# Optimization experiments

Measured on AMD Instinct MI355X. Metric: run time of the kernel, lower is better.

## Reference

```python
import jax, jax.numpy as jnp
import numpy as np

L, B, D, H = 4096, 4, 1024, 16
HD = D // H
SCALAR = 700.0


def setup_inputs() -> dict:
    key = jax.random.key(0)
    ks = jax.random.split(key, 9)
    bound = np.sqrt(6.0 / (D + D)).astype(np.float32)  # xavier_uniform for square weights
    def xavier(k):
        return jax.random.uniform(k, (D, D), jnp.float32, -bound, bound)
    return {
        "input_tensor": jax.random.normal(ks[0], (L, B, D), jnp.float32),
        "num_heads": H,
        "Wq": xavier(ks[1]), "bq": jnp.zeros((D,), jnp.float32),
        "Wk": xavier(ks[2]), "bk": jnp.zeros((D,), jnp.float32),
        "Wv": xavier(ks[3]), "bv": jnp.zeros((D,), jnp.float32),
        "Wo": xavier(ks[4]), "bo": jnp.zeros((D,), jnp.float32),
        "scalar": jnp.asarray(SCALAR, jnp.float32),
    }


def reference(input_tensor, num_heads, Wq, bq, Wk, bk, Wv, bv, Wo, bo, scalar):
    l, b, d = input_tensor.shape
    h = num_heads
    hd = d // h
    scaling = hd ** -0.5
    X = jnp.transpose(input_tensor, (1, 0, 2))  # (b, l, d)
    q = (X @ Wq.T + bq) * scaling
    k = X @ Wk.T + bk
    v = X @ Wv.T + bv
    # split heads: (b, l, h*hd) -> (b, h, l, hd)
    q = q.reshape(b, l, h, hd).transpose(0, 2, 1, 3)
    k = k.reshape(b, l, h, hd).transpose(0, 2, 1, 3)
    v = v.reshape(b, l, h, hd).transpose(0, 2, 1, 3)
    # linear attention: (K^T V) then Q @ (...)  -> O(l * hd^2)
    kv = jnp.einsum('bhld,bhle->bhde', k, v)        # (b, h, hd, hd)
    out = jnp.einsum('bhld,bhde->bhle', q, kv) / scalar  # (b, h, l, hd)
    # faithful to einops '(b h) l d -> b l (d h)': feature layout is (hd, h)
    out = out.transpose(0, 2, 3, 1).reshape(b, l, d)  # (b, l, hd*h)
    out = out @ Wo.T + bo
    return jnp.transpose(out, (1, 0, 2))  # (l, b, d)
```

## Files before the change

### kernel.cpp

```cpp
#include <hip/hip_runtime.h>
#include <stdint.h>
#include <stddef.h>

typedef unsigned short ushort_t;
typedef __attribute__((ext_vector_type(8))) short short8;
typedef __attribute__((ext_vector_type(4))) float f32x4;
typedef __attribute__((ext_vector_type(4))) float float4v;

#define L_DIM 4096
#define B_DIM 4
#define D_DIM 1024
#define H_DIM 16
#define HD_DIM 64
#define M_DIM (L_DIM * B_DIM)

__device__ __forceinline__ float bf2f(ushort_t u) {
    union { unsigned int i; float f; } v; v.i = ((unsigned int)u) << 16; return v.f;
}
__device__ __forceinline__ ushort_t f2bf(float f) {
    union { float f; unsigned int i; } v; v.f = f;
    unsigned int r = v.i + 0x7FFFu + ((v.i >> 16) & 1u);
    return (ushort_t)(r >> 16);
}
__device__ __forceinline__ unsigned int pk2(float a, float b) {
    return (unsigned int)f2bf(a) | ((unsigned int)f2bf(b) << 16);
}
__device__ __forceinline__ void gload16(const ushort_t* g, ushort_t* l) {
    __builtin_amdgcn_global_load_lds(
        (const __attribute__((address_space(1))) unsigned int*)g,
        (__attribute__((address_space(3))) unsigned int*)l, 16, 0, 0);
}

__global__ void detect_kernel(const ushort_t* __restrict__ scal, int* __restrict__ flag)
{
    *flag = (scal[0] == 0) ? 1 : 0;
}

__global__ void convert_b_kernel(const void* bq, const void* bk, const void* bv,
                                 const void* bo, float* __restrict__ bias_f,
                                 const int* __restrict__ flag)
{
    int fl = *flag;
    int idx = blockIdx.x * 256 + threadIdx.x;
    int j = idx >> 10, i = idx & 1023;
    const void* p = (j == 0) ? bq : (j == 1) ? bk : (j == 2) ? bv : bo;
    bias_f[idx] = fl ? ((const float*)p)[i] : bf2f(((const ushort_t*)p)[i]);
}

__global__ void convert_w_kernel(const void* Wk, const void* Wv, const void* Wo,
                                 ushort_t* __restrict__ Wkc, ushort_t* __restrict__ Wvc,
                                 ushort_t* __restrict__ Wpc,
                                 const int* __restrict__ flag)
{
    int fl = *flag;
    int z = blockIdx.z;
    int idx = blockIdx.x * 256 + threadIdx.x;
    const void* src = (z == 0) ? Wk : (z == 1) ? Wv : Wo;
    ushort_t* dst   = (z == 0) ? Wkc : (z == 1) ? Wvc : Wpc;
    size_t sidx;
    if (z < 2) sidx = (size_t)idx;
    else {
        int n = idx >> 10, f = idx & 1023;
        int hh = f >> 6, e = f & 63;
        sidx = (size_t)n * D_DIM + e * H_DIM + hh;
    }
    dst[idx] = fl ? f2bf(((const float*)src)[sidx]) : ((const ushort_t*)src)[sidx];
}

__global__ void convert_x_kernel(const void* __restrict__ X, ushort_t* __restrict__ Xb,
                                 const int* __restrict__ flag)
{
    int fl = *flag;
    size_t i8 = ((size_t)blockIdx.x * 256 + threadIdx.x) * 8;
    if (fl) {
        const float4v* p = (const float4v*)((const float*)X + i8);
        float4v f0 = p[0], f1 = p[1];
        uint4 u;
        u.x = pk2(f0.x, f0.y); u.y = pk2(f0.z, f0.w);
        u.z = pk2(f1.x, f1.y); u.w = pk2(f1.z, f1.w);
        *(uint4*)(Xb + i8) = u;
    } else {
        *(uint4*)(Xb + i8) = *(const uint4*)((const ushort_t*)X + i8);
    }
}

__global__ __launch_bounds__(256) void proj_kernel(
    const ushort_t* __restrict__ A, int a_base0, int a_zstride, int astride,
    const ushort_t* __restrict__ W0, int w_z,
    const float* __restrict__ bias0, int b_z,
    void* __restrict__ out, int o_base0, int o_zstride, int ostride,
    const int* __restrict__ flag, int o_dyn)
{
    __shared__ ushort_t lA[128 * 32];
    __shared__ ushort_t lB[128 * 32];
    const int z    = blockIdx.z;
    const int a_base = a_base0 + z * a_zstride;
    const int o_base = o_base0 + z * o_zstride;
    const ushort_t* W = W0 + (size_t)z * w_z * (D_DIM * D_DIM);
    const float* bias = bias0 + z * b_z * D_DIM;
    const int ofl  = o_dyn & *flag;
    const int t    = threadIdx.x;
    const int m0   = blockIdx.x * 128;
    const int n0   = blockIdx.y * 128;
    const int w    = t >> 6;
    const int lane = t & 63;
    const int quad = lane >> 4;
    const int l16  = lane & 15;
    const int wm   = (w >> 1) * 64;
    const int wn   = (w & 1) * 64;

    const int c0 = t, c1 = t + 256;
    const int r0 = c0 >> 2, col0 = (c0 & 3) * 8;
    const int r1 = c1 >> 2, col1 = (c1 & 3) * 8;

    f32x4 acc[4][4];
#pragma unroll
    for (int i = 0; i < 4; i++)
#pragma unroll
        for (int j = 0; j < 4; j++) acc[i][j] = f32x4{0.f, 0.f, 0.f, 0.f};

    for (int k0 = 0; k0 < D_DIM; k0 += 32) {
        __syncthreads();
        gload16(A + (size_t)(a_base + (m0 + r0) * astride) * D_DIM + k0 + col0, &lA[c0 * 8]);
        gload16(A + (size_t)(a_base + (m0 + r1) * astride) * D_DIM + k0 + col1, &lA[c1 * 8]);
        gload16(W + (size_t)(n0 + r0) * D_DIM + k0 + col0, &lB[c0 * 8]);
        gload16(W + (size_t)(n0 + r1) * D_DIM + k0 + col1, &lB[c1 * 8]);
        __syncthreads();
        short8 af[4], bfr[4];
#pragma unroll
        for (int mt = 0; mt < 4; mt++)
            af[mt] = *(const short8*)&lA[(wm + mt * 16 + l16) * 32 + quad * 8];
#pragma unroll
        for (int nt = 0; nt < 4; nt++)
            bfr[nt] = *(const short8*)&lB[(wn + nt * 16 + l16) * 32 + quad * 8];
#pragma unroll
        for (int mt = 0; mt < 4; mt++)
#pragma unroll
            for (int nt = 0; nt < 4; nt++)
                acc[mt][nt] = __builtin_amdgcn_mfma_f32_16x16x32_bf16(
                    af[mt], bfr[nt], acc[mt][nt], 0, 0, 0);
    }

#pragma unroll
    for (int mt = 0; mt < 4; mt++) {
#pragma unroll
        for (int nt = 0; nt < 4; nt++) {
            int gn = n0 + wn + nt * 16 + l16;
            float bv = bias[gn];
#pragma unroll
            for (int i = 0; i < 4; i++) {
                int gm = m0 + wm + mt * 16 + quad * 4 + i;
                size_t oidx = (size_t)(o_base + gm * ostride) * D_DIM + gn;
                float val = acc[mt][nt][i] + bv;
                if (ofl) ((float*)out)[oidx] = val;
                else     ((ushort_t*)out)[oidx] = f2bf(val);
            }
        }
    }
}

__global__ __launch_bounds__(256) void kv_chunk_kernel(
    const ushort_t* __restrict__ kc, const ushort_t* __restrict__ vc,
    float* __restrict__ part, int lps)
{
    __shared__ ushort_t lkT[64 * 32];
    __shared__ ushort_t lvT[64 * 32];
    const int t    = threadIdx.x;
    const int s    = blockIdx.x;
    const int bh   = blockIdx.y;
    const int b    = bh >> 4, h = bh & 15;
    const int w    = t >> 6;
    const int lane = t & 63, quad = lane >> 4, l16 = lane & 15;

    f32x4 acc[4];
#pragma unroll
    for (int i = 0; i < 4; i++) acc[i] = f32x4{0.f, 0.f, 0.f, 0.f};

    const int niter = lps >> 5;
    for (int kt = 0; kt < niter; kt++) {
        int lcur = s * lps + kt * 32;
        __syncthreads();
#pragma unroll
        for (int i = 0; i < 4; i++) {
            int u  = t + 256 * i;
            int l  = u >> 5;
            int dp = u & 31;
            size_t goff = ((size_t)(lcur + l) * B_DIM + b) * D_DIM + h * HD_DIM + dp * 2;
            unsigned int kw = *(const unsigned int*)(kc + goff);
            unsigned int vw = *(const unsigned int*)(vc + goff);
            lkT[(2 * dp) * 32 + l]     = (ushort_t)kw;
            lkT[(2 * dp + 1) * 32 + l] = (ushort_t)(kw >> 16);
            lvT[(2 * dp) * 32 + l]     = (ushort_t)vw;
            lvT[(2 * dp + 1) * 32 + l] = (ushort_t)(vw >> 16);
        }
        __syncthreads();
        short8 af = *(const short8*)&lvT[(w * 16 + l16) * 32 + quad * 8];
#pragma unroll
        for (int dt = 0; dt < 4; dt++) {
            short8 bfr = *(const short8*)&lkT[(dt * 16 + l16) * 32 + quad * 8];
            acc[dt] = __builtin_amdgcn_mfma_f32_16x16x32_bf16(af, bfr, acc[dt], 0, 0, 0);
        }
    }
#pragma unroll
    for (int dt = 0; dt < 4; dt++) {
#pragma unroll
        for (int i = 0; i < 4; i++) {
            int e = w * 16 + quad * 4 + i;
            int d = dt * 16 + l16;
            part[(((size_t)s * 64 + bh) * 64 + e) * 64 + d] += acc[dt][i];
        }
    }
}

__global__ void kv_reduce_kernel(const float* __restrict__ part,
                                 ushort_t* __restrict__ kvT,
                                 const void* __restrict__ scal,
                                 const int* __restrict__ flag)
{
    int fl = *flag;
    float sc = fl ? *(const float*)scal : bf2f(((const ushort_t*)scal)[0]);
    float inv = 1.0f / sc;
    int idx = blockIdx.x * 256 + threadIdx.x;
    float sum = 0.0f;
#pragma unroll
    for (int s = 0; s < 4; s++) sum += part[((size_t)s << 18) + idx];
    kvT[idx] = f2bf(sum * inv);
}

__global__ __launch_bounds__(256) void wfuse_kernel(
    const void* __restrict__ Wq, const ushort_t* __restrict__ kvT,
    ushort_t* __restrict__ Wf, const int* __restrict__ flag)
{
    __shared__ ushort_t kvL[4096];
    const int fl = *flag;
    const int kt = blockIdx.x, h = blockIdx.y, b = blockIdx.z;
    const int t  = threadIdx.x;
    for (int i = t; i < 2048; i += 256)
        ((unsigned int*)kvL)[i] =
            ((const unsigned int*)(kvT + ((size_t)(b * 16 + h) << 12)))[i];
    __syncthreads();
    const int k  = kt * 128 + (t & 127);
    const int e0 = (t >> 7) * 32;
    float acc[32];
#pragma unroll
    for (int j = 0; j < 32; j++) acc[j] = 0.f;
    for (int d = 0; d < 64; d++) {
        size_t wi = (size_t)(h * 64 + d) * D_DIM + k;
        float wv = 0.125f * (fl ? ((const float*)Wq)[wi]
                                : bf2f(((const ushort_t*)Wq)[wi]));
#pragma unroll
        for (int j = 0; j < 32; j++)
            acc[j] += bf2f(kvL[(e0 + j) * 64 + d]) * wv;
    }
#pragma unroll
    for (int j = 0; j < 32; j++)
        Wf[((size_t)b * 1024 + h * 64 + e0 + j) * D_DIM + k] = f2bf(acc[j]);
}

__global__ void bias_fuse_kernel(const float* __restrict__ bq_f,
                                 const ushort_t* __restrict__ kvT,
                                 float* __restrict__ bfused)
{
    int idx = blockIdx.x * 256 + threadIdx.x;
    int b = idx >> 10, h = (idx >> 6) & 15, e = idx & 63;
    const ushort_t* kvp = kvT + ((size_t)(b * 16 + h) << 12) + e * 64;
    float s = 0.f;
#pragma unroll
    for (int d = 0; d < 64; d++) s += bf2f(kvp[d]) * bq_f[h * 64 + d];
    bfused[idx] = 0.125f * s;
}

extern "C" void kernel_launch(void* const* d_in, const int* in_sizes, int n_in,
                              void* d_out, int out_size, void* d_ws, size_t ws_size,
                              hipStream_t stream)
{
    const void* X    = d_in[0];
    const void* Wq   = d_in[2];
    const void* bq   = d_in[3];
    const void* Wk   = d_in[4];
    const void* bk   = d_in[5];
    const void* Wv   = d_in[6];
    const void* bv   = d_in[7];
    const void* Wo   = d_in[8];
    const void* bo   = d_in[9];
    const void* scal = d_in[10];

    char* ws = (char*)d_ws;
    int*      flag   = (int*)(ws + 0);
    float*    bias_f = (float*)(ws + 1024);
    float*    bfused = (float*)(ws + 32768);
    ushort_t* Wkc    = (ushort_t*)(ws + 65536);
    ushort_t* Wvc    = (ushort_t*)(ws + 2162688);
    ushort_t* Wpc    = (ushort_t*)(ws + 4259840);
    ushort_t* Wfused = (ushort_t*)(ws + 6356992);
    ushort_t* kvT    = (ushort_t*)(ws + 14745600);
    float*    part   = (float*)(ws + 15269888);
    ushort_t* Xb     = (ushort_t*)(ws + 19464192);
    ushort_t* kvbuf  = (ushort_t*)(ws + 53018624);
    ushort_t* kc     = kvbuf;
    ushort_t* vc     = kvbuf + (size_t)8192 * D_DIM;
    ushort_t* attnb  = kvbuf;

    detect_kernel<<<1, 1, 0, stream>>>((const ushort_t*)scal, flag);
    convert_b_kernel<<<16, 256, 0, stream>>>(bq, bk, bv, bo, bias_f, flag);
    convert_w_kernel<<<dim3(4096, 1, 3), 256, 0, stream>>>(Wk, Wv, Wo, Wkc, Wvc, Wpc, flag);
    convert_x_kernel<<<8192, 256, 0, stream>>>(X, Xb, flag);
    hipMemsetAsync(part, 0, 4194304, stream);

    for (int c = 0; c < 2; c++) {
        proj_kernel<<<dim3(64, 8, 2), 256, 0, stream>>>(
            Xb, c * 8192, 0, 1,
            Wkc, 1,
            bias_f + 1024, 1,
            kvbuf, 0, 8192, 1,
            flag, 0);
        kv_chunk_kernel<<<dim3(4, 64), 256, 0, stream>>>(kc, vc, part, 512);
    }
    kv_reduce_kernel<<<1024, 256, 0, stream>>>(part, kvT, scal, flag);

    wfuse_kernel<<<dim3(8, 16, 4), 256, 0, stream>>>(Wq, kvT, Wfused, flag);
    bias_fuse_kernel<<<16, 256, 0, stream>>>(bias_f, kvT, bfused);

    proj_kernel<<<dim3(32, 8, 4), 256, 0, stream>>>(
        Xb, 0, 1, 4,
        Wfused, 1,
        bfused, 1,
        attnb, 0, 4096, 1,
        flag, 0);

    proj_kernel<<<dim3(32, 8, 4), 256, 0, stream>>>(
        attnb, 0, 4096, 1,
        Wpc, 0,
        bias_f + 3072, 0,
        d_out, 0, 1, 4,
        flag, 1);
}
```

Before: 488.0 us.

## Fold output projection into fused Q weight, eliminating one full-size GEMM

The per-batch fused query weight (Wq scaled and combined with KV) is now multiplied by Wo up front in a small 1024x1024 per-batch GEMM. A single large projection of X then produces the output directly, with a matching fused bias computed by a new bias2 kernel. This removes one 16384x1024x1024 GEMM and the intermediate attention buffer, at the cost of a small extra weight GEMM, an extra bf16 rounding step on the combined weight, and a transposed wfuse store pattern. The KV chunk split is also doubled from 4 to 8 partial sums, with a larger partial buffer and reduction.

```diff
diff --git a/kernel.cpp b/kernel.cpp
--- a/kernel.cpp
+++ b/kernel.cpp
@@ -223,13 +223,13 @@
     int idx = blockIdx.x * 256 + threadIdx.x;
     float sum = 0.0f;
 #pragma unroll
-    for (int s = 0; s < 4; s++) sum += part[((size_t)s << 18) + idx];
+    for (int s = 0; s < 8; s++) sum += part[((size_t)s << 18) + idx];
     kvT[idx] = f2bf(sum * inv);
 }
 
 __global__ __launch_bounds__(256) void wfuse_kernel(
     const void* __restrict__ Wq, const ushort_t* __restrict__ kvT,
-    ushort_t* __restrict__ Wf, const int* __restrict__ flag)
+    ushort_t* __restrict__ WfT, const int* __restrict__ flag)
 {
     __shared__ ushort_t kvL[4096];
     const int fl = *flag;
@@ -254,7 +254,7 @@
     }
 #pragma unroll
     for (int j = 0; j < 32; j++)
-        Wf[((size_t)b * 1024 + h * 64 + e0 + j) * D_DIM + k] = f2bf(acc[j]);
+        WfT[((size_t)b * 1024 + k) * D_DIM + h * 64 + e0 + j] = f2bf(acc[j]);
 }
 
 __global__ void bias_fuse_kernel(const float* __restrict__ bq_f,
@@ -268,6 +268,20 @@
 #pragma unroll
     for (int d = 0; d < 64; d++) s += bf2f(kvp[d]) * bq_f[h * 64 + d];
     bfused[idx] = 0.125f * s;
+}
+
+__global__ void bias2_kernel(const ushort_t* __restrict__ Wpc,
+                             const float* __restrict__ bfused,
+                             const float* __restrict__ bo_f,
+                             float* __restrict__ b2)
+{
+    int idx = blockIdx.x * 256 + threadIdx.x;
+    int b = idx >> 10, n = idx & 1023;
+    const ushort_t* wr = Wpc + (size_t)n * D_DIM;
+    const float* bf = bfused + b * 1024;
+    float s = 0.f;
+    for (int f = 0; f < 1024; f++) s += bf2f(wr[f]) * bf[f];
+    b2[idx] = s + bo_f[n];
 }
 
 extern "C" void kernel_launch(void* const* d_in, const int* in_sizes, int n_in,
@@ -289,23 +303,26 @@
     int*      flag   = (int*)(ws + 0);
     float*    bias_f = (float*)(ws + 1024);
     float*    bfused = (float*)(ws + 32768);
-    ushort_t* Wkc    = (ushort_t*)(ws + 65536);
-    ushort_t* Wvc    = (ushort_t*)(ws + 2162688);
-    ushort_t* Wpc    = (ushort_t*)(ws + 4259840);
-    ushort_t* Wfused = (ushort_t*)(ws + 6356992);
-    ushort_t* kvT    = (ushort_t*)(ws + 14745600);
-    float*    part   = (float*)(ws + 15269888);
-    ushort_t* Xb     = (ushort_t*)(ws + 19464192);
-    ushort_t* kvbuf  = (ushort_t*)(ws + 53018624);
+    float*    b2     = (float*)(ws + 65536);
+    float*    bias_z = (float*)(ws + 98304);
+    ushort_t* Wkc    = (ushort_t*)(ws + 131072);
+    ushort_t* Wvc    = (ushort_t*)(ws + 2228224);
+    ushort_t* Wpc    = (ushort_t*)(ws + 4325376);
+    ushort_t* kvT    = (ushort_t*)(ws + 6422528);
+    float*    part   = (float*)(ws + 6946816);
+    ushort_t* Xb     = (ushort_t*)(ws + 15335424);
+    ushort_t* kvbuf  = (ushort_t*)(ws + 48889856);
     ushort_t* kc     = kvbuf;
     ushort_t* vc     = kvbuf + (size_t)8192 * D_DIM;
-    ushort_t* attnb  = kvbuf;
+    ushort_t* WfT    = kvbuf;
+    ushort_t* W2     = kvbuf + (size_t)4194304;
 
     detect_kernel<<<1, 1, 0, stream>>>((const ushort_t*)scal, flag);
     convert_b_kernel<<<16, 256, 0, stream>>>(bq, bk, bv, bo, bias_f, flag);
     convert_w_kernel<<<dim3(4096, 1, 3), 256, 0, stream>>>(Wk, Wv, Wo, Wkc, Wvc, Wpc, flag);
     convert_x_kernel<<<8192, 256, 0, stream>>>(X, Xb, flag);
-    hipMemsetAsync(part, 0, 4194304, stream);
+    hipMemsetAsync(part, 0, 8388608, stream);
+    hipMemsetAsync(bias_z, 0, 4096, stream);
 
     for (int c = 0; c < 2; c++) {
         proj_kernel<<<dim3(64, 8, 2), 256, 0, stream>>>(
@@ -314,24 +331,25 @@
             bias_f + 1024, 1,
             kvbuf, 0, 8192, 1,
             flag, 0);
-        kv_chunk_kernel<<<dim3(4, 64), 256, 0, stream>>>(kc, vc, part, 512);
+        kv_chunk_kernel<<<dim3(8, 64), 256, 0, stream>>>(kc, vc, part, 256);
     }
     kv_reduce_kernel<<<1024, 256, 0, stream>>>(part, kvT, scal, flag);
 
-    wfuse_kernel<<<dim3(8, 16, 4), 256, 0, stream>>>(Wq, kvT, Wfused, flag);
+    wfuse_kernel<<<dim3(8, 16, 4), 256, 0, stream>>>(Wq, kvT, WfT, flag);
     bias_fuse_kernel<<<16, 256, 0, stream>>>(bias_f, kvT, bfused);
+    bias2_kernel<<<16, 256, 0, stream>>>(Wpc, bfused, bias_f + 3072, b2);
+
+    proj_kernel<<<dim3(8, 8, 4), 256, 0, stream>>>(
+        Wpc, 0, 0, 1,
+        WfT, 1,
+        bias_z, 0,
+        W2, 0, 1024, 1,
+        flag, 0);
 
     proj_kernel<<<dim3(32, 8, 4), 256, 0, stream>>>(
         Xb, 0, 1, 4,
-        Wfused, 1,
-        bfused, 1,
-        attnb, 0, 4096, 1,
-        flag, 0);
-
-    proj_kernel<<<dim3(32, 8, 4), 256, 0, stream>>>(
-        attnb, 0, 4096, 1,
-        Wpc, 0,
-        bias_f + 3072, 0,
+        W2, 1,
+        b2, 1,
         d_out, 0, 1, 4,
         flag, 1);
 }
```

After: 487.1 us. Within noise of the previous version (-0.2%).
